# Optimization experiments

Measured on AMD Instinct MI355X. Metric: run time of the kernel, lower is better.

The kernel has to match this reference:

```python
import jax, jax.numpy as jnp
import numpy as np

B, S, D, H = 64, 64, 4096, 64  # NOTE: code requires S == H (see notes)
HD = D // H  # 64


def setup_inputs() -> dict:
    key = jax.random.key(0)
    ks = jax.random.split(key, 9)
    std = 0.02
    return {
        "x": jax.random.normal(ks[0], (B, S, D), dtype=jnp.float32),
        "Wq": jax.random.normal(ks[1], (D, D), dtype=jnp.float32) * std,
        "bq": jax.random.normal(ks[2], (D,), dtype=jnp.float32) * std,
        "Wk": jax.random.normal(ks[3], (D, D), dtype=jnp.float32) * std,
        "bk": jax.random.normal(ks[4], (D,), dtype=jnp.float32) * std,
        "Wv": jax.random.normal(ks[5], (D, D), dtype=jnp.float32) * std,
        "bv": jax.random.normal(ks[6], (D,), dtype=jnp.float32) * std,
        "Wp": jax.random.normal(ks[7], (D, D), dtype=jnp.float32) * std,
        "bp": jax.random.normal(ks[8], (D,), dtype=jnp.float32) * std,
    }


def reference(x, Wq, bq, Wk, bk, Wv, bv, Wp, bp):
    b, s, d = x.shape
    h, hd = H, d // H
    # q, k: [B,S,D] -> [B,S,H,hd] -> [B,H,S,hd]
    q = (x @ Wq.T + bq).reshape(b, s, h, hd).transpose(0, 2, 1, 3)
    k = (x @ Wk.T + bk).reshape(b, s, h, hd).transpose(0, 2, 1, 3)
    # v: faithfully replicates the original buggy view(B, H, S, hd).transpose(1,2)
    # -> shape [B, S, H, hd] (NOT head-major)
    v = (x @ Wv.T + bv).reshape(b, h, s, hd).transpose(0, 2, 1, 3)
    # attention WITHOUT 1/sqrt(hd) scaling (faithful to source)
    attn = jax.nn.softmax(jnp.einsum("bhqd,bhkd->bhqk", q, k), axis=-1)  # [B,H,S,S]
    # dropout layers are identity in eval mode
    # ShardedTensor: chunk v along last dim into 2 shards of hd/2
    v0, v1 = jnp.split(v, 2, axis=-1)  # each [B,S,H,hd/2]; broadcast needs S==H
    out0 = jnp.matmul(attn, v0)  # [B,H,S,hd/2]
    out1 = jnp.matmul(attn, v1)
    out = jnp.concatenate([out0, out1], axis=0)  # [2B,H,S,hd/2] (faithful cat on dim 0)
    out = out.transpose(0, 2, 1, 3).reshape(b, s, d)  # row-major regroup, same as torch view
    return out @ Wp.T + bp
```

## Files before the change

kernel.cpp:

```cpp
#include <hip/hip_runtime.h>
#include <stdint.h>

typedef __bf16   bf16x8  __attribute__((ext_vector_type(8)));
typedef float    f32x4   __attribute__((ext_vector_type(4)));
typedef uint16_t u16x8   __attribute__((ext_vector_type(8)));

using as1_cvp = const __attribute__((address_space(1))) void*;
using as3_vp  = __attribute__((address_space(3))) void*;

__device__ __forceinline__ uint16_t f2bf(float f) {
    uint32_t u = __float_as_uint(f);
    u += 0x7FFF + ((u >> 16) & 1);
    return (uint16_t)(u >> 16);
}

__device__ __forceinline__ void gload16(const void* g, void* l) {
    __builtin_amdgcn_global_load_lds((as1_cvp)g, (as3_vp)l, 16, 0, 0);
}

#define MFMA16(a, b, c) __builtin_amdgcn_mfma_f32_16x16x32_bf16((a), (b), (c), 0, 0, 0)

__global__ __launch_bounds__(256)
void cvt_bf16(const float* __restrict__ in, uint16_t* __restrict__ out, int n8)
{
    int i = blockIdx.x * 256 + threadIdx.x;
    if (i >= n8) return;
    const float4* p = reinterpret_cast<const float4*>(in) + (size_t)i * 2;
    float4 a = p[0], b = p[1];
    u16x8 o;
    o[0] = f2bf(a.x); o[1] = f2bf(a.y); o[2] = f2bf(a.z); o[3] = f2bf(a.w);
    o[4] = f2bf(b.x); o[5] = f2bf(b.y); o[6] = f2bf(b.z); o[7] = f2bf(b.w);
    reinterpret_cast<u16x8*>(out)[i] = o;
}

__global__ __launch_bounds__(256)
void cvt5(const float* __restrict__ s0, const float* __restrict__ s1,
          const float* __restrict__ s2, const float* __restrict__ s3,
          const float* __restrict__ s4,
          uint16_t* __restrict__ d0, uint16_t* __restrict__ d1,
          uint16_t* __restrict__ d2, uint16_t* __restrict__ d3,
          uint16_t* __restrict__ d4)
{
    const int r = blockIdx.x >> 13;
    const float*  src = (r == 0) ? s0 : (r == 1) ? s1 : (r == 2) ? s2
                       : (r == 3) ? s3 : s4;
    uint16_t*     dst = (r == 0) ? d0 : (r == 1) ? d1 : (r == 2) ? d2
                       : (r == 3) ? d3 : d4;
    const int i = (blockIdx.x & 8191) * 256 + threadIdx.x;
    const float4* p = reinterpret_cast<const float4*>(src) + (size_t)i * 2;
    float4 a = p[0], b = p[1];
    u16x8 o;
    o[0] = f2bf(a.x); o[1] = f2bf(a.y); o[2] = f2bf(a.z); o[3] = f2bf(a.w);
    o[4] = f2bf(b.x); o[5] = f2bf(b.y); o[6] = f2bf(b.z); o[7] = f2bf(b.w);
    reinterpret_cast<u16x8*>(dst)[i] = o;
}

template <int OUT_BF16>
__global__ __launch_bounds__(512, 2)
void gemm256(const uint16_t* __restrict__ A, const uint16_t* __restrict__ Bt,
             const float* __restrict__ bias, void* __restrict__ Cout,
             int M, int N, int K)
{
    __shared__ uint16_t lds[65536];
    const int NT = K >> 6;

    int bid = blockIdx.x;
    bid = (bid & 7) * 32 + (bid >> 3);
    const int bx = bid & 15, by = bid >> 4;
    const int rb = by * 256, cb = bx * 256;

    const int tid  = threadIdx.x;
    const int w    = tid >> 6;
    const int lane = tid & 63;
    const int g    = lane >> 4;
    const int l16  = lane & 15;
    const int wm   = w >> 2;
    const int wn   = w & 3;
    const int srow = lane >> 2;
    const int sblk = lane & 3;

    f32x4 acc[8][4] = {};

    auto stageA = [&](int buf, int kh, int kbase) {
#pragma unroll
        for (int i = 0; i < 2; ++i) {
            const int row = i * 128 + w * 16 + srow;
            const uint16_t* src = A + (size_t)(rb + row) * K + kbase
                                    + ((sblk ^ ((row >> 1) & 3)) << 3);
            gload16(src, &lds[(buf * 2 + kh) * 16384 + i * 4096 + w * 512]);
        }
    };
    auto stageB = [&](int buf, int kh, int kbase) {
#pragma unroll
        for (int i = 0; i < 2; ++i) {
            const int row = i * 128 + w * 16 + srow;
            const uint16_t* src = Bt + (size_t)(cb + row) * K + kbase
                                     + ((sblk ^ ((row >> 1) & 3)) << 3);
            gload16(src, &lds[(buf * 2 + kh) * 16384 + 8192 + i * 4096 + w * 512]);
        }
    };

    auto readA = [&](int base, int grp, bf16x8* dst) {
#pragma unroll
        for (int mi = 0; mi < 4; ++mi) {
            const int r = wm * 128 + grp * 64 + mi * 16 + l16;
            dst[mi] = *reinterpret_cast<const bf16x8*>(
                &lds[base + r * 32 + ((g ^ ((r >> 1) & 3)) << 3)]);
        }
    };
    auto readB = [&](int base, bf16x8* dst) {
#pragma unroll
        for (int n = 0; n < 4; ++n) {
            const int c = wn * 64 + n * 16 + l16;
            dst[n] = *reinterpret_cast<const bf16x8*>(
                &lds[base + 8192 + c * 32 + ((g ^ ((c >> 1) & 3)) << 3)]);
        }
    };

    auto mfma_grp = [&](int grp, const bf16x8* af, const bf16x8* bf) {
        __builtin_amdgcn_s_setprio(1);
#pragma unroll
        for (int mi = 0; mi < 4; ++mi)
#pragma unroll
            for (int n = 0; n < 4; ++n)
                acc[grp * 4 + mi][n] = MFMA16(af[mi], bf[n], acc[grp * 4 + mi][n]);
        __builtin_amdgcn_s_setprio(0);
    };

    stageA(0, 0, 0);  stageB(0, 0, 0);
    stageA(0, 1, 32); stageB(0, 1, 32);
    stageA(1, 0, 64); stageB(1, 0, 64);
    asm volatile("s_waitcnt vmcnt(4)" ::: "memory");
    __builtin_amdgcn_s_barrier();

    for (int t = 0; t < NT; ++t) {
        const int cur = t & 1, nxt = cur ^ 1;
        const int b0 = (cur * 2 + 0) * 16384;
        const int b1 = (cur * 2 + 1) * 16384;
        bf16x8 af0[4], af1[4], af2[4], af3[4], bf0[4], bf1[4];

        if (t + 1 < NT) stageA(nxt, 1, (t + 1) * 64 + 32);
        readA(b0, 0, af0); readB(b0, bf0);
        readA(b0, 1, af1);
        mfma_grp(0, af0, bf0);
        __builtin_amdgcn_sched_barrier(0);
        __builtin_amdgcn_s_barrier();

        if (t + 1 < NT) stageB(nxt, 1, (t + 1) * 64 + 32);
        readB(b1, bf1);
        readA(b1, 0, af2);
        mfma_grp(1, af1, bf0);
        __builtin_amdgcn_sched_barrier(0);
        __builtin_amdgcn_s_barrier();

        if (t + 2 < NT) stageA(cur, 0, (t + 2) * 64);
        readA(b1, 1, af3);
        mfma_grp(0, af2, bf1);
        __builtin_amdgcn_sched_barrier(0);
        __builtin_amdgcn_s_barrier();

        if (t + 2 < NT) stageB(cur, 0, (t + 2) * 64);
        mfma_grp(1, af3, bf1);
        __builtin_amdgcn_sched_barrier(0);
        if (t >= NT - 2) asm volatile("s_waitcnt vmcnt(0)" ::: "memory");
        else             asm volatile("s_waitcnt vmcnt(4)" ::: "memory");
        __builtin_amdgcn_s_barrier();
    }

    float bv[4];
#pragma unroll
    for (int n = 0; n < 4; ++n) bv[n] = bias[cb + wn * 64 + n * 16 + l16];

#pragma unroll
    for (int m = 0; m < 8; ++m) {
#pragma unroll
        for (int n = 0; n < 4; ++n) {
            const int col = cb + wn * 64 + n * 16 + l16;
#pragma unroll
            for (int r = 0; r < 4; ++r) {
                const int row = rb + wm * 128 + m * 16 + g * 4 + r;
                float v = acc[m][n][r] + bv[n];
                if (OUT_BF16)
                    ((uint16_t*)Cout)[(size_t)row * N + col] = f2bf(v);
                else
                    ((float*)Cout)[(size_t)row * N + col] = v;
            }
        }
    }
}

__global__ __launch_bounds__(256)
void attn_kernel(const uint16_t* __restrict__ Q, const uint16_t* __restrict__ Kg,
                 const uint16_t* __restrict__ V, uint16_t* __restrict__ Y)
{
    const int bid = blockIdx.x;
    const int hh  = bid & 63;
    const int bb  = bid >> 6;
    const int tid = threadIdx.x;
    const int w   = tid >> 6, lane = tid & 63, g = lane >> 4, l16 = lane & 15;

    __shared__ uint16_t Vt[64 * 64];
    __shared__ uint16_t Pl[64 * 64];

    {
        const int k  = tid >> 2;
        const int l0 = (tid & 3) * 16;
        const uint16_t* src = V + (size_t)(bb * 64 + k) * 4096 + hh * 64 + l0;
        u16x8 v0 = *reinterpret_cast<const u16x8*>(src);
        u16x8 v1 = *reinterpret_cast<const u16x8*>(src + 8);
#pragma unroll
        for (int i = 0; i < 8; ++i) {
            int l = l0 + i;
            Vt[l * 64 + (k ^ ((l & 7) << 3))] = v0[i];
        }
#pragma unroll
        for (int i = 0; i < 8; ++i) {
            int l = l0 + 8 + i;
            Vt[l * 64 + (k ^ ((l & 7) << 3))] = v1[i];
        }
    }

    f32x4 sa[4] = {};
    {
        const uint16_t* qrow = Q + (size_t)(bb * 64 + w * 16 + l16) * 4096 + hh * 64 + g * 8;
        bf16x8 a0 = *reinterpret_cast<const bf16x8*>(qrow);
        bf16x8 a1 = *reinterpret_cast<const bf16x8*>(qrow + 32);
#pragma unroll
        for (int n = 0; n < 4; ++n) {
            const uint16_t* krow = Kg + (size_t)(bb * 64 + n * 16 + l16) * 4096 + hh * 64 + g * 8;
            bf16x8 b0 = *reinterpret_cast<const bf16x8*>(krow);
            bf16x8 b1 = *reinterpret_cast<const bf16x8*>(krow + 32);
            sa[n] = MFMA16(a0, b0, sa[n]);
            sa[n] = MFMA16(a1, b1, sa[n]);
        }
    }

    float p[4][4];
#pragma unroll
    for (int j = 0; j < 4; ++j) {
        float mx = fmaxf(fmaxf(sa[0][j], sa[1][j]), fmaxf(sa[2][j], sa[3][j]));
        mx = fmaxf(mx, __shfl_xor(mx, 1));
        mx = fmaxf(mx, __shfl_xor(mx, 2));
        mx = fmaxf(mx, __shfl_xor(mx, 4));
        mx = fmaxf(mx, __shfl_xor(mx, 8));
        float s = 0.f;
#pragma unroll
        for (int n = 0; n < 4; ++n) { p[n][j] = __expf(sa[n][j] - mx); s += p[n][j]; }
        s += __shfl_xor(s, 1);
        s += __shfl_xor(s, 2);
        s += __shfl_xor(s, 4);
        s += __shfl_xor(s, 8);
        float inv = 1.0f / s;
#pragma unroll
        for (int n = 0; n < 4; ++n) p[n][j] *= inv;
    }

#pragma unroll
    for (int j = 0; j < 4; ++j) {
        const int q = w * 16 + g * 4 + j;
#pragma unroll
        for (int n = 0; n < 4; ++n) {
            const int kcol = n * 16 + l16;
            Pl[q * 64 + (kcol ^ ((q & 7) << 3))] = f2bf(p[n][j]);
        }
    }
    __syncthreads();

    f32x4 oa[4] = {};
    {
        const int qr = w * 16 + l16;
        bf16x8 a0 = *reinterpret_cast<const bf16x8*>(&Pl[qr * 64 + ((g * 8)      ^ ((qr & 7) << 3))]);
        bf16x8 a1 = *reinterpret_cast<const bf16x8*>(&Pl[qr * 64 + ((32 + g * 8) ^ ((qr & 7) << 3))]);
#pragma unroll
        for (int n = 0; n < 4; ++n) {
            const int vr = n * 16 + l16;
            bf16x8 b0 = *reinterpret_cast<const bf16x8*>(&Vt[vr * 64 + ((g * 8)      ^ ((vr & 7) << 3))]);
            bf16x8 b1 = *reinterpret_cast<const bf16x8*>(&Vt[vr * 64 + ((32 + g * 8) ^ ((vr & 7) << 3))]);
            oa[n] = MFMA16(a0, b0, oa[n]);
            oa[n] = MFMA16(a1, b1, oa[n]);
        }
    }

#pragma unroll
    for (int n = 0; n < 4; ++n) {
        const int ll = n * 16 + l16;
#pragma unroll
        for (int r = 0; r < 4; ++r) {
            const int qq = w * 16 + g * 4 + r;
            const int b_ = (bb >> 1) + ((ll >= 32) ? 32 : 0);
            const int s_ = ((bb & 1) << 5) + (qq >> 1);
            const int h_ = ((qq & 1) << 5) + (hh >> 1);
            const int l_ = ((hh & 1) << 5) + (ll & 31);
            Y[(size_t)(b_ * 64 + s_) * 4096 + h_ * 64 + l_] = f2bf(oa[n][r]);
        }
    }
}

extern "C" void kernel_launch(void* const* d_in, const int* in_sizes, int n_in,
                              void* d_out, int out_size, void* d_ws, size_t ws_size,
                              hipStream_t stream)
{
    (void)in_sizes; (void)n_in; (void)out_size;

    const float* x  = (const float*)d_in[0];
    const float* Wq = (const float*)d_in[1];
    const float* bq = (const float*)d_in[2];
    const float* Wk = (const float*)d_in[3];
    const float* bk = (const float*)d_in[4];
    const float* Wv = (const float*)d_in[5];
    const float* bv = (const float*)d_in[6];
    const float* Wp = (const float*)d_in[7];
    const float* bp = (const float*)d_in[8];
    float* out = (float*)d_out;

    const size_t NN = 16777216;
    const int n8 = (int)(NN / 8);
    dim3 cgrid((n8 + 255) / 256), cblk(256);
    dim3 ggrid(256), gblk(512);

    if (ws_size >= NN * 2 * 8) {
        uint16_t* xb  = (uint16_t*)d_ws;
        uint16_t* wqb = xb  + NN;
        uint16_t* wkb = wqb + NN;
        uint16_t* wvb = wkb + NN;
        uint16_t* wpb = wvb + NN;
        uint16_t* Qb  = wpb + NN;
        uint16_t* Kb  = Qb  + NN;
        uint16_t* Vb  = Kb  + NN;
        uint16_t* Yb  = xb;

        cvt5<<<dim3(8192 * 5), cblk, 0, stream>>>(x, Wq, Wk, Wv, Wp,
                                                  xb, wqb, wkb, wvb, wpb);
        gemm256<1><<<ggrid, gblk, 0, stream>>>(xb, wqb, bq, (void*)Qb, 4096, 4096, 4096);
        gemm256<1><<<ggrid, gblk, 0, stream>>>(xb, wkb, bk, (void*)Kb, 4096, 4096, 4096);
        gemm256<1><<<ggrid, gblk, 0, stream>>>(xb, wvb, bv, (void*)Vb, 4096, 4096, 4096);
        attn_kernel<<<dim3(4096), dim3(256), 0, stream>>>(Qb, Kb, Vb, Yb);
        gemm256<0><<<ggrid, gblk, 0, stream>>>(Yb, wpb, bp, (void*)out, 4096, 4096, 4096);
    } else {
        uint16_t* xb = (uint16_t*)d_ws;
        uint16_t* wb = xb + NN;
        uint16_t* Qb = wb + NN;
        uint16_t* Kb = Qb + NN;
        uint16_t* Vb = Kb + NN;
        uint16_t* Yb = xb;

        cvt_bf16<<<cgrid, cblk, 0, stream>>>(x, xb, n8);
        cvt_bf16<<<cgrid, cblk, 0, stream>>>(Wq, wb, n8);
        gemm256<1><<<ggrid, gblk, 0, stream>>>(xb, wb, bq, (void*)Qb, 4096, 4096, 4096);
        cvt_bf16<<<cgrid, cblk, 0, stream>>>(Wk, wb, n8);
        gemm256<1><<<ggrid, gblk, 0, stream>>>(xb, wb, bk, (void*)Kb, 4096, 4096, 4096);
        cvt_bf16<<<cgrid, cblk, 0, stream>>>(Wv, wb, n8);
        gemm256<1><<<ggrid, gblk, 0, stream>>>(xb, wb, bv, (void*)Vb, 4096, 4096, 4096);
        attn_kernel<<<dim3(4096), dim3(256), 0, stream>>>(Qb, Kb, Vb, Yb);
        cvt_bf16<<<cgrid, cblk, 0, stream>>>(Wp, wb, n8);
        gemm256<0><<<ggrid, gblk, 0, stream>>>(Yb, wb, bp, (void*)out, 4096, 4096, 4096);
    }
}
```

Measured before the change: 599.8 us.

## Shrink GEMM tile from 256x256 to 128x128 with four-wave blocks

Replaces the 256x256-tile, 512-thread GEMM with a 128x128-tile, 256-thread variant launched on a 1024-block grid. LDS use is halved and the inner loop is simplified to two MFMA groups per K step with combined A/B staging. The aim is to fill more of the device's compute units with four times as many blocks. The cost is lower arithmetic intensity per tile (more global/L2 traffic) and a less interleaved load/compute schedule.

```diff
diff --git a/kernel.cpp b/kernel.cpp
--- a/kernel.cpp
+++ b/kernel.cpp
@@ -56,54 +56,54 @@
 }
 
 template <int OUT_BF16>
-__global__ __launch_bounds__(512, 2)
-void gemm256(const uint16_t* __restrict__ A, const uint16_t* __restrict__ Bt,
+__global__ __launch_bounds__(256, 2)
+void gemm128(const uint16_t* __restrict__ A, const uint16_t* __restrict__ Bt,
              const float* __restrict__ bias, void* __restrict__ Cout,
              int M, int N, int K)
 {
-    __shared__ uint16_t lds[65536];
+    __shared__ uint16_t lds[32768];
     const int NT = K >> 6;
 
     int bid = blockIdx.x;
-    bid = (bid & 7) * 32 + (bid >> 3);
-    const int bx = bid & 15, by = bid >> 4;
-    const int rb = by * 256, cb = bx * 256;
+    bid = (bid & 7) * 128 + (bid >> 3);
+    const int bx = bid & 31, by = bid >> 5;
+    const int rb = by * 128, cb = bx * 128;
 
     const int tid  = threadIdx.x;
     const int w    = tid >> 6;
     const int lane = tid & 63;
     const int g    = lane >> 4;
     const int l16  = lane & 15;
-    const int wm   = w >> 2;
-    const int wn   = w & 3;
+    const int wm   = w >> 1;
+    const int wn   = w & 1;
     const int srow = lane >> 2;
     const int sblk = lane & 3;
 
-    f32x4 acc[8][4] = {};
+    f32x4 acc[4][4] = {};
 
     auto stageA = [&](int buf, int kh, int kbase) {
 #pragma unroll
         for (int i = 0; i < 2; ++i) {
-            const int row = i * 128 + w * 16 + srow;
+            const int row = i * 64 + w * 16 + srow;
             const uint16_t* src = A + (size_t)(rb + row) * K + kbase
                                     + ((sblk ^ ((row >> 1) & 3)) << 3);
-            gload16(src, &lds[(buf * 2 + kh) * 16384 + i * 4096 + w * 512]);
+            gload16(src, &lds[(buf * 2 + kh) * 8192 + i * 2048 + w * 512]);
         }
     };
     auto stageB = [&](int buf, int kh, int kbase) {
 #pragma unroll
         for (int i = 0; i < 2; ++i) {
-            const int row = i * 128 + w * 16 + srow;
+            const int row = i * 64 + w * 16 + srow;
             const uint16_t* src = Bt + (size_t)(cb + row) * K + kbase
                                      + ((sblk ^ ((row >> 1) & 3)) << 3);
-            gload16(src, &lds[(buf * 2 + kh) * 16384 + 8192 + i * 4096 + w * 512]);
-        }
-    };
-
-    auto readA = [&](int base, int grp, bf16x8* dst) {
+            gload16(src, &lds[(buf * 2 + kh) * 8192 + 4096 + i * 2048 + w * 512]);
+        }
+    };
+
+    auto readA = [&](int base, bf16x8* dst) {
 #pragma unroll
         for (int mi = 0; mi < 4; ++mi) {
-            const int r = wm * 128 + grp * 64 + mi * 16 + l16;
+            const int r = wm * 64 + mi * 16 + l16;
             dst[mi] = *reinterpret_cast<const bf16x8*>(
                 &lds[base + r * 32 + ((g ^ ((r >> 1) & 3)) << 3)]);
         }
@@ -113,17 +113,17 @@
         for (int n = 0; n < 4; ++n) {
             const int c = wn * 64 + n * 16 + l16;
             dst[n] = *reinterpret_cast<const bf16x8*>(
-                &lds[base + 8192 + c * 32 + ((g ^ ((c >> 1) & 3)) << 3)]);
-        }
-    };
-
-    auto mfma_grp = [&](int grp, const bf16x8* af, const bf16x8* bf) {
+                &lds[base + 4096 + c * 32 + ((g ^ ((c >> 1) & 3)) << 3)]);
+        }
+    };
+
+    auto mfma16 = [&](const bf16x8* af, const bf16x8* bf) {
         __builtin_amdgcn_s_setprio(1);
 #pragma unroll
         for (int mi = 0; mi < 4; ++mi)
 #pragma unroll
             for (int n = 0; n < 4; ++n)
-                acc[grp * 4 + mi][n] = MFMA16(af[mi], bf[n], acc[grp * 4 + mi][n]);
+                acc[mi][n] = MFMA16(af[mi], bf[n], acc[mi][n]);
         __builtin_amdgcn_s_setprio(0);
     };
 
@@ -135,32 +135,21 @@
 
     for (int t = 0; t < NT; ++t) {
         const int cur = t & 1, nxt = cur ^ 1;
-        const int b0 = (cur * 2 + 0) * 16384;
-        const int b1 = (cur * 2 + 1) * 16384;
-        bf16x8 af0[4], af1[4], af2[4], af3[4], bf0[4], bf1[4];
-
-        if (t + 1 < NT) stageA(nxt, 1, (t + 1) * 64 + 32);
-        readA(b0, 0, af0); readB(b0, bf0);
-        readA(b0, 1, af1);
-        mfma_grp(0, af0, bf0);
+        const int b0 = (cur * 2 + 0) * 8192;
+        const int b1 = (cur * 2 + 1) * 8192;
+        bf16x8 af0[4], bf0[4], af1[4], bf1[4];
+
+        if (t + 1 < NT) { stageA(nxt, 1, (t + 1) * 64 + 32);
+                          stageB(nxt, 1, (t + 1) * 64 + 32); }
+        readA(b0, af0); readB(b0, bf0);
+        readA(b1, af1); readB(b1, bf1);
+        mfma16(af0, bf0);
         __builtin_amdgcn_sched_barrier(0);
         __builtin_amdgcn_s_barrier();
 
-        if (t + 1 < NT) stageB(nxt, 1, (t + 1) * 64 + 32);
-        readB(b1, bf1);
-        readA(b1, 0, af2);
-        mfma_grp(1, af1, bf0);
-        __builtin_amdgcn_sched_barrier(0);
-        __builtin_amdgcn_s_barrier();
-
-        if (t + 2 < NT) stageA(cur, 0, (t + 2) * 64);
-        readA(b1, 1, af3);
-        mfma_grp(0, af2, bf1);
-        __builtin_amdgcn_sched_barrier(0);
-        __builtin_amdgcn_s_barrier();
-
-        if (t + 2 < NT) stageB(cur, 0, (t + 2) * 64);
-        mfma_grp(1, af3, bf1);
+        if (t + 2 < NT) { stageA(cur, 0, (t + 2) * 64);
+                          stageB(cur, 0, (t + 2) * 64); }
+        mfma16(af1, bf1);
         __builtin_amdgcn_sched_barrier(0);
         if (t >= NT - 2) asm volatile("s_waitcnt vmcnt(0)" ::: "memory");
         else             asm volatile("s_waitcnt vmcnt(4)" ::: "memory");
@@ -172,13 +161,13 @@
     for (int n = 0; n < 4; ++n) bv[n] = bias[cb + wn * 64 + n * 16 + l16];
 
 #pragma unroll
-    for (int m = 0; m < 8; ++m) {
+    for (int m = 0; m < 4; ++m) {
 #pragma unroll
         for (int n = 0; n < 4; ++n) {
             const int col = cb + wn * 64 + n * 16 + l16;
 #pragma unroll
             for (int r = 0; r < 4; ++r) {
-                const int row = rb + wm * 128 + m * 16 + g * 4 + r;
+                const int row = rb + wm * 64 + m * 16 + g * 4 + r;
                 float v = acc[m][n][r] + bv[n];
                 if (OUT_BF16)
                     ((uint16_t*)Cout)[(size_t)row * N + col] = f2bf(v);
@@ -316,7 +305,7 @@
     const size_t NN = 16777216;
     const int n8 = (int)(NN / 8);
     dim3 cgrid((n8 + 255) / 256), cblk(256);
-    dim3 ggrid(256), gblk(512);
+    dim3 ggrid(1024), gblk(256);
 
     if (ws_size >= NN * 2 * 8) {
         uint16_t* xb  = (uint16_t*)d_ws;
@@ -331,11 +320,11 @@
 
         cvt5<<<dim3(8192 * 5), cblk, 0, stream>>>(x, Wq, Wk, Wv, Wp,
                                                   xb, wqb, wkb, wvb, wpb);
-        gemm256<1><<<ggrid, gblk, 0, stream>>>(xb, wqb, bq, (void*)Qb, 4096, 4096, 4096);
-        gemm256<1><<<ggrid, gblk, 0, stream>>>(xb, wkb, bk, (void*)Kb, 4096, 4096, 4096);
-        gemm256<1><<<ggrid, gblk, 0, stream>>>(xb, wvb, bv, (void*)Vb, 4096, 4096, 4096);
+        gemm128<1><<<ggrid, gblk, 0, stream>>>(xb, wqb, bq, (void*)Qb, 4096, 4096, 4096);
+        gemm128<1><<<ggrid, gblk, 0, stream>>>(xb, wkb, bk, (void*)Kb, 4096, 4096, 4096);
+        gemm128<1><<<ggrid, gblk, 0, stream>>>(xb, wvb, bv, (void*)Vb, 4096, 4096, 4096);
         attn_kernel<<<dim3(4096), dim3(256), 0, stream>>>(Qb, Kb, Vb, Yb);
-        gemm256<0><<<ggrid, gblk, 0, stream>>>(Yb, wpb, bp, (void*)out, 4096, 4096, 4096);
+        gemm128<0><<<ggrid, gblk, 0, stream>>>(Yb, wpb, bp, (void*)out, 4096, 4096, 4096);
     } else {
         uint16_t* xb = (uint16_t*)d_ws;
         uint16_t* wb = xb + NN;
@@ -346,13 +335,13 @@
 
         cvt_bf16<<<cgrid, cblk, 0, stream>>>(x, xb, n8);
         cvt_bf16<<<cgrid, cblk, 0, stream>>>(Wq, wb, n8);
-        gemm256<1><<<ggrid, gblk, 0, stream>>>(xb, wb, bq, (void*)Qb, 4096, 4096, 4096);
+        gemm128<1><<<ggrid, gblk, 0, stream>>>(xb, wb, bq, (void*)Qb, 4096, 4096, 4096);
         cvt_bf16<<<cgrid, cblk, 0, stream>>>(Wk, wb, n8);
-        gemm256<1><<<ggrid, gblk, 0, stream>>>(xb, wb, bk, (void*)Kb, 4096, 4096, 4096);
+        gemm128<1><<<ggrid, gblk, 0, stream>>>(xb, wb, bk, (void*)Kb, 4096, 4096, 4096);
         cvt_bf16<<<cgrid, cblk, 0, stream>>>(Wv, wb, n8);
-        gemm256<1><<<ggrid, gblk, 0, stream>>>(xb, wb, bv, (void*)Vb, 4096, 4096, 4096);
+        gemm128<1><<<ggrid, gblk, 0, stream>>>(xb, wb, bv, (void*)Vb, 4096, 4096, 4096);
         attn_kernel<<<dim3(4096), dim3(256), 0, stream>>>(Qb, Kb, Vb, Yb);
         cvt_bf16<<<cgrid, cblk, 0, stream>>>(Wp, wb, n8);
-        gemm256<0><<<ggrid, gblk, 0, stream>>>(Yb, wb, bp, (void*)out, 4096, 4096, 4096);
-    }
-}
+        gemm128<0><<<ggrid, gblk, 0, stream>>>(Yb, wb, bp, (void*)out, 4096, 4096, 4096);
+    }
+}
```

After: 816.3 us. 1.36x slower.
